# Kernel tuning notes

Measured on AMD Instinct MI355X. Metric: run time of the kernel, lower is better.

Reference implementation:

```python
import jax, jax.numpy as jnp
import numpy as np

N, D_IN, D_OUT = 8192, 1024, 1024

def setup_inputs() -> dict:
    key = jax.random.key(0)
    kx, kq, kk, kv = jax.random.split(key, 4)
    s = 1.0 / np.sqrt(D_IN)
    return {
        "x": jax.random.normal(kx, (N, D_IN), dtype=jnp.float32),
        "W_q": jax.random.normal(kq, (D_OUT, D_IN), dtype=jnp.float32) * s,
        "W_k": jax.random.normal(kk, (D_OUT, D_IN), dtype=jnp.float32) * s,
        "W_v": jax.random.normal(kv, (D_OUT, D_IN), dtype=jnp.float32) * s,
    }

def reference(x, W_q, W_k, W_v):
    # nn.Linear stores weight as [out, in]: y = x @ W.T
    q = x @ W_q.T          # [N, D_OUT]
    k = x @ W_k.T          # [N, D_OUT]
    v = x @ W_v.T          # [N, D_OUT]
    scale = 1.0 / jnp.sqrt(jnp.asarray(k.shape[-1], dtype=x.dtype))
    scores = (q @ k.T) * scale            # [N, N]
    attn = jax.nn.softmax(scores, axis=-1)
    return attn @ v                        # [N, D_OUT]
```

## Files before the change

### kernel.cpp

```cpp
#include <hip/hip_runtime.h>
#include <hip/hip_bf16.h>
#include <cstdint>
#include <cstddef>


typedef __attribute__((ext_vector_type(8))) short short8;
typedef __attribute__((ext_vector_type(8))) unsigned short ushort8;
typedef __attribute__((ext_vector_type(4))) float f32x4;

#define FENCE asm volatile("" ::: "memory")

__device__ __forceinline__ unsigned short f2bf(float f) {
  unsigned u = __float_as_uint(f);
  u += 0x7fffu + ((u >> 16) & 1u);
  return (unsigned short)(u >> 16);
}
__device__ __forceinline__ float bf2f(unsigned short h) {
  return __uint_as_float(((unsigned)h) << 16);
}

__device__ __forceinline__ void glds16(const void* g, void* l) {
  __builtin_amdgcn_global_load_lds((__attribute__((address_space(1))) void*)g,
                                   (__attribute__((address_space(3))) void*)l,
                                   16, 0, 0);
}

__global__ __launch_bounds__(256) void cast_kernel(const float* __restrict__ in,
                                                   unsigned short* __restrict__ out,
                                                   int n8) {
  int i = blockIdx.x * 256 + threadIdx.x;
  if (i >= n8) return;
  const f32x4* in4 = (const f32x4*)in;
  f32x4 a = in4[2 * i];
  f32x4 b = in4[2 * i + 1];
  ushort8 o;
#pragma unroll
  for (int j = 0; j < 4; ++j) o[j] = f2bf(a[j]);
#pragma unroll
  for (int j = 0; j < 4; ++j) o[4 + j] = f2bf(b[j]);
  ((ushort8*)out)[i] = o;
}

#define MFMA_OP(mi, ni, av, bv) \
  acc[mi][ni] = __builtin_amdgcn_mfma_f32_16x16x32_bf16(av, bv, acc[mi][ni], 0, 0, 0)

template <typename OutT>
__device__ __forceinline__ void gemm_core(
    const unsigned short* __restrict__ A, const unsigned short* __restrict__ B,
    OutT* __restrict__ C, int ldc, size_t ldab , int NT,
    int gm0, int gn0, float scale, char* lA, char* lB) {
  const int tid = threadIdx.x;
  const int lane = tid & 63, w = tid >> 6;
  const int wm = w >> 2, wn = w & 3;

  const int rc0 = w * 32 + (lane >> 2);
  const int rc1 = rc0 + 16;
  const int scol = ((lane & 3) << 4) ^ (((lane >> 3) & 3) << 4);
  const char* pA0 = (const char*)A + (size_t)(gm0 + rc0) * ldab + scol;
  const char* pA1 = (const char*)A + (size_t)(gm0 + rc1) * ldab + scol;
  const char* pB0 = (const char*)B + (size_t)(gn0 + rc0) * ldab + scol;
  const char* pB1 = (const char*)B + (size_t)(gn0 + rc1) * ldab + scol;
  char* dA = lA + w * 2048;
  char* dB = lB + w * 2048;

  const int colb = ((lane >> 4) << 4) ^ (((lane >> 1) & 3) << 4);
  const int aoff = (wm * 128 + (lane & 15)) * 64 + colb;
  const int boff = (wn * 64 + (lane & 15)) * 64 + colb;

  f32x4 acc[8][4];
#pragma unroll
  for (int m = 0; m < 8; ++m)
#pragma unroll
    for (int n = 0; n < 4; ++n) acc[m][n] = (f32x4)(0.0f);

  for (int t = 0; t < 2; ++t) {
    glds16(pA0 + (size_t)t * 64, dA + t * 16384);
    glds16(pA1 + (size_t)t * 64, dA + t * 16384 + 1024);
    glds16(pB0 + (size_t)t * 64, dB + t * 16384);
    glds16(pB1 + (size_t)t * 64, dB + t * 16384 + 1024);
  }
  asm volatile("s_waitcnt vmcnt(4)" ::: "memory");
  __builtin_amdgcn_s_barrier();
  FENCE;

  for (int t = 0; t < NT; ++t) {
    const int slot = t & 3;
    const char* As = lA + slot * 16384;
    const char* Bs = lB + slot * 16384;
    const bool stg = (t + 2 < NT);
    const int s2 = (t + 2) & 3;
    const size_t go = (size_t)(t + 2) * 64;
    short8 a0, a1, a2, a3, b0, b1, b2, b3;

    if (stg) glds16(pA0 + go, dA + s2 * 16384);
    a0 = *(const short8*)(As + aoff);
    a1 = *(const short8*)(As + aoff + 1024);
    a2 = *(const short8*)(As + aoff + 2048);
    a3 = *(const short8*)(As + aoff + 3072);
    b0 = *(const short8*)(Bs + boff);
    b1 = *(const short8*)(Bs + boff + 1024);
    __builtin_amdgcn_s_setprio(1);
    MFMA_OP(0, 0, a0, b0); MFMA_OP(0, 1, a0, b1);
    MFMA_OP(1, 0, a1, b0); MFMA_OP(1, 1, a1, b1);
    MFMA_OP(2, 0, a2, b0); MFMA_OP(2, 1, a2, b1);
    MFMA_OP(3, 0, a3, b0); MFMA_OP(3, 1, a3, b1);
    __builtin_amdgcn_s_setprio(0);
    FENCE; __builtin_amdgcn_s_barrier(); FENCE;

    if (stg) glds16(pA1 + go, dA + s2 * 16384 + 1024);
    b2 = *(const short8*)(Bs + boff + 2048);
    b3 = *(const short8*)(Bs + boff + 3072);
    __builtin_amdgcn_s_setprio(1);
    MFMA_OP(0, 2, a0, b2); MFMA_OP(0, 3, a0, b3);
    MFMA_OP(1, 2, a1, b2); MFMA_OP(1, 3, a1, b3);
    MFMA_OP(2, 2, a2, b2); MFMA_OP(2, 3, a2, b3);
    MFMA_OP(3, 2, a3, b2); MFMA_OP(3, 3, a3, b3);
    __builtin_amdgcn_s_setprio(0);
    FENCE; __builtin_amdgcn_s_barrier(); FENCE;

    if (stg) glds16(pB0 + go, dB + s2 * 16384);
    a0 = *(const short8*)(As + aoff + 4096);
    a1 = *(const short8*)(As + aoff + 5120);
    a2 = *(const short8*)(As + aoff + 6144);
    a3 = *(const short8*)(As + aoff + 7168);
    __builtin_amdgcn_s_setprio(1);
    MFMA_OP(4, 0, a0, b0); MFMA_OP(4, 1, a0, b1);
    MFMA_OP(5, 0, a1, b0); MFMA_OP(5, 1, a1, b1);
    MFMA_OP(6, 0, a2, b0); MFMA_OP(6, 1, a2, b1);
    MFMA_OP(7, 0, a3, b0); MFMA_OP(7, 1, a3, b1);
    __builtin_amdgcn_s_setprio(0);
    FENCE; __builtin_amdgcn_s_barrier(); FENCE;

    if (stg) glds16(pB1 + go, dB + s2 * 16384 + 1024);
    __builtin_amdgcn_s_setprio(1);
    MFMA_OP(4, 2, a0, b2); MFMA_OP(4, 3, a0, b3);
    MFMA_OP(5, 2, a1, b2); MFMA_OP(5, 3, a1, b3);
    MFMA_OP(6, 2, a2, b2); MFMA_OP(6, 3, a2, b3);
    MFMA_OP(7, 2, a3, b2); MFMA_OP(7, 3, a3, b3);
    __builtin_amdgcn_s_setprio(0);
    if (stg) asm volatile("s_waitcnt vmcnt(4)" ::: "memory");
    else     asm volatile("s_waitcnt vmcnt(0)" ::: "memory");
    __builtin_amdgcn_s_barrier();
    FENCE;
  }

  const int r0 = gm0 + wm * 128 + ((lane >> 4) << 2);
  const int c0 = gn0 + wn * 64 + (lane & 15);
#pragma unroll
  for (int mi = 0; mi < 8; ++mi) {
#pragma unroll
    for (int ni = 0; ni < 4; ++ni) {
      f32x4 v = acc[mi][ni];
#pragma unroll
      for (int j = 0; j < 4; ++j) {
        float val = v[j] * scale;
        size_t idx = (size_t)(r0 + mi * 16 + j) * ldc + (c0 + ni * 16);
        if (sizeof(OutT) == 2) ((unsigned short*)C)[idx] = f2bf(val);
        else                   ((float*)C)[idx] = val;
      }
    }
  }
}

__device__ __forceinline__ void swz_block(int& bx, int& by, int& bz) {
  const int gx = gridDim.x, gy = gridDim.y;
  const int f = (blockIdx.z * gy + blockIdx.y) * gx + blockIdx.x;
  const int nwg = gx * gy * gridDim.z;
  const int q = nwg >> 3;
  const int l = (f & 7) * q + (f >> 3);
  bx = l % gx;
  const int r = l / gx;
  by = r % gy;
  bz = r / gy;
}

__global__ __launch_bounds__(512, 2) void gemm_s_kernel(
    const unsigned short* __restrict__ Q, const unsigned short* __restrict__ Kh,
    unsigned short* __restrict__ S) {
  __shared__ char lA[4 * 16384];
  __shared__ char lB[4 * 16384];
  int bx, by, bz; swz_block(bx, by, bz);
  gemm_core<unsigned short>(Q, Kh, S, 8192, 2048, 32, by * 256, bx * 256,
                            0.03125f, lA, lB);
}

__global__ __launch_bounds__(512, 2) void gemm_qkv_kernel(
    const unsigned short* __restrict__ X,
    const unsigned short* __restrict__ Wq, const unsigned short* __restrict__ Wk,
    const unsigned short* __restrict__ Wv,
    unsigned short* __restrict__ Qo, unsigned short* __restrict__ Ko,
    unsigned short* __restrict__ Vo) {
  __shared__ char lA[4 * 16384];
  __shared__ char lB[4 * 16384];
  int bx, by, bz; swz_block(bx, by, bz);
  const unsigned short* B = (bz == 0) ? Wq : (bz == 1) ? Wk : Wv;
  unsigned short* C = (bz == 0) ? Qo : (bz == 1) ? Ko : Vo;
  gemm_core<unsigned short>(X, B, C, 1024, 2048, 32, by * 256, bx * 256,
                            1.0f, lA, lB);
}

__global__ __launch_bounds__(512, 2) void gemm_pv_kernel(
    const unsigned short* __restrict__ S, const unsigned short* __restrict__ Vt,
    float* __restrict__ O, float* __restrict__ P1) {
  __shared__ char lA[4 * 16384];
  __shared__ char lB[4 * 16384];
  int bx, by, bz; swz_block(bx, by, bz);
  const unsigned short* A = S + (size_t)bz * 4096;
  const unsigned short* B = Vt + (size_t)bz * 4096;
  float* C = bz ? P1 : O;
  gemm_core<float>(A, B, C, 1024, 16384, 128, by * 256, bx * 256, 1.0f, lA, lB);
}

__global__ __launch_bounds__(256) void add_kernel(float* __restrict__ out,
                                                  const float* __restrict__ p,
                                                  int n4) {
  int i = blockIdx.x * 256 + threadIdx.x;
  if (i < n4) {
    f32x4 a = ((const f32x4*)out)[i];
    f32x4 b = ((const f32x4*)p)[i];
    ((f32x4*)out)[i] = a + b;
  }
}

__global__ __launch_bounds__(256) void softmax_kernel(unsigned short* __restrict__ S,
                                                      int ncol) {
  const int t = threadIdx.x;
  unsigned short* rp = S + (size_t)blockIdx.x * ncol;
  ushort8* rv = (ushort8*)rp;
  float f[32];
#pragma unroll
  for (int c = 0; c < 4; ++c) {
    ushort8 v = rv[c * 256 + t];
#pragma unroll
    for (int j = 0; j < 8; ++j) f[c * 8 + j] = bf2f(v[j]);
  }
  float m = -1e30f;
#pragma unroll
  for (int i = 0; i < 32; ++i) m = fmaxf(m, f[i]);
#pragma unroll
  for (int o = 32; o; o >>= 1) m = fmaxf(m, __shfl_xor(m, o));
  __shared__ float red[8];
  if ((t & 63) == 0) red[t >> 6] = m;
  __syncthreads();
  m = fmaxf(fmaxf(red[0], red[1]), fmaxf(red[2], red[3]));

  float s = 0.0f;
#pragma unroll
  for (int i = 0; i < 32; ++i) {
    f[i] = __expf(f[i] - m);
    s += f[i];
  }
#pragma unroll
  for (int o = 32; o; o >>= 1) s += __shfl_xor(s, o);
  if ((t & 63) == 0) red[4 + (t >> 6)] = s;
  __syncthreads();
  s = red[4] + red[5] + red[6] + red[7];
  float inv = 1.0f / s;
#pragma unroll
  for (int c = 0; c < 4; ++c) {
    ushort8 v;
#pragma unroll
    for (int j = 0; j < 8; ++j) v[j] = f2bf(f[c * 8 + j] * inv);
    rv[c * 256 + t] = v;
  }
}

__global__ __launch_bounds__(256) void transpose_kernel(
    const unsigned short* __restrict__ in, unsigned short* __restrict__ out,
    int R, int Ccols) {
  __shared__ unsigned short tile[64][65];
  const int tx = threadIdx.x & 63, ty = threadIdx.x >> 6;
  const int r0 = blockIdx.y * 64, c0 = blockIdx.x * 64;
#pragma unroll
  for (int i = 0; i < 16; ++i) {
    int r = ty * 16 + i;
    tile[r][tx] = in[(size_t)(r0 + r) * Ccols + c0 + tx];
  }
  __syncthreads();
#pragma unroll
  for (int i = 0; i < 16; ++i) {
    int r = ty * 16 + i;
    out[(size_t)(c0 + r) * R + r0 + tx] = tile[tx][r];
  }
}

extern "C" void kernel_launch(void* const* d_in, const int* in_sizes, int n_in,
                              void* d_out, int out_size, void* d_ws, size_t ws_size,
                              hipStream_t stream) {
  (void)in_sizes; (void)n_in; (void)out_size; (void)ws_size;
  const int N = 8192, D = 1024;
  const float* x  = (const float*)d_in[0];
  const float* Wq = (const float*)d_in[1];
  const float* Wk = (const float*)d_in[2];
  const float* Wv = (const float*)d_in[3];
  float* out = (float*)d_out;

  char* ws = (char*)d_ws;
  size_t off = 0;
  auto alloc = [&](size_t bytes) { char* p = ws + off; off += bytes; return p; };
  unsigned short* xh  = (unsigned short*)alloc((size_t)N * D * 2);
  unsigned short* Wqh = (unsigned short*)alloc((size_t)D * D * 2);
  unsigned short* Wkh = (unsigned short*)alloc((size_t)D * D * 2);
  unsigned short* Wvh = (unsigned short*)alloc((size_t)D * D * 2);
  unsigned short* Qh  = (unsigned short*)alloc((size_t)N * D * 2);
  unsigned short* Kh  = (unsigned short*)alloc((size_t)N * D * 2);
  unsigned short* Vh  = (unsigned short*)alloc((size_t)N * D * 2);
  unsigned short* S   = (unsigned short*)alloc((size_t)N * N * 2);
  unsigned short* Vth = xh;
  float* Pbuf = (float*)Qh;

  cast_kernel<<<(N * D / 8) / 256, 256, 0, stream>>>(x, xh, N * D / 8);
  cast_kernel<<<(D * D / 8) / 256, 256, 0, stream>>>(Wq, Wqh, D * D / 8);
  cast_kernel<<<(D * D / 8) / 256, 256, 0, stream>>>(Wk, Wkh, D * D / 8);
  cast_kernel<<<(D * D / 8) / 256, 256, 0, stream>>>(Wv, Wvh, D * D / 8);

  gemm_qkv_kernel<<<dim3(4, 32, 3), 512, 0, stream>>>(xh, Wqh, Wkh, Wvh,
                                                      Qh, Kh, Vh);

  gemm_s_kernel<<<dim3(32, 32), 512, 0, stream>>>(Qh, Kh, S);

  softmax_kernel<<<N, 256, 0, stream>>>(S, N);

  transpose_kernel<<<dim3(D / 64, N / 64), 256, 0, stream>>>(Vh, Vth, N, D);

  gemm_pv_kernel<<<dim3(4, 32, 2), 512, 0, stream>>>(S, Vth, out, Pbuf);

  add_kernel<<<(N * D / 4) / 256, 256, 0, stream>>>(out, Pbuf, N * D / 4);
}
```

Baseline: 608.9 us.

## Double-buffer 64-wide K tiles with register-prefetched fragments in GEMM core

Reworks the shared GEMM main loop to stage K-tiles of 64 instead of 32, using two LDS buffers of 64 KB each (128 KB total) with a new XOR swizzle. A and B fragments are held in registers in lo/hi halves, and the next A fragment is prefetched before the final MFMA quad. This halves the number of outer iterations and the barrier overhead per K element. The S-GEMM output is also written with nontemporal stores so the large score matrix bypasses cache. In exchange the kernel uses much more LDS, which may rule out two blocks per CU despite launch_bounds(512,2), and adds register pressure and extra barriers.

```diff
diff --git a/kernel.cpp b/kernel.cpp
--- a/kernel.cpp
+++ b/kernel.cpp
@@ -9,6 +9,9 @@
 typedef __attribute__((ext_vector_type(4))) float f32x4;
 
 #define FENCE asm volatile("" ::: "memory")
+__device__ __forceinline__ void wgbar() {
+  FENCE; __builtin_amdgcn_s_barrier(); FENCE;
+}
 
 __device__ __forceinline__ unsigned short f2bf(float f) {
   unsigned u = __float_as_uint(f);
@@ -41,31 +44,40 @@
   ((ushort8*)out)[i] = o;
 }
 
-#define MFMA_OP(mi, ni, av, bv) \
-  acc[mi][ni] = __builtin_amdgcn_mfma_f32_16x16x32_bf16(av, bv, acc[mi][ni], 0, 0, 0)
-
-template <typename OutT>
+#define QUAD(mbase, nbase, aArr, bArr)                                        \
+  do {                                                                        \
+    _Pragma("unroll") for (int m_ = 0; m_ < 4; ++m_)                          \
+    _Pragma("unroll") for (int n_ = 0; n_ < 2; ++n_)                          \
+    _Pragma("unroll") for (int k_ = 0; k_ < 2; ++k_)                          \
+      acc[(mbase) + m_][(nbase) + n_] =                                       \
+        __builtin_amdgcn_mfma_f32_16x16x32_bf16(aArr[m_][k_], bArr[n_][k_],   \
+          acc[(mbase) + m_][(nbase) + n_], 0, 0, 0);                          \
+  } while (0)
+
+template <typename OutT, bool NTS>
 __device__ __forceinline__ void gemm_core(
     const unsigned short* __restrict__ A, const unsigned short* __restrict__ B,
-    OutT* __restrict__ C, int ldc, size_t ldab , int NT,
-    int gm0, int gn0, float scale, char* lA, char* lB) {
+    OutT* __restrict__ C, int ldc, size_t ldab , int NT2,
+    int gm0, int gn0, float scale, char* lds) {
   const int tid = threadIdx.x;
   const int lane = tid & 63, w = tid >> 6;
   const int wm = w >> 2, wn = w & 3;
 
-  const int rc0 = w * 32 + (lane >> 2);
-  const int rc1 = rc0 + 16;
-  const int scol = ((lane & 3) << 4) ^ (((lane >> 3) & 3) << 4);
-  const char* pA0 = (const char*)A + (size_t)(gm0 + rc0) * ldab + scol;
-  const char* pA1 = (const char*)A + (size_t)(gm0 + rc1) * ldab + scol;
-  const char* pB0 = (const char*)B + (size_t)(gn0 + rc0) * ldab + scol;
-  const char* pB1 = (const char*)B + (size_t)(gn0 + rc1) * ldab + scol;
-  char* dA = lA + w * 2048;
-  char* dB = lB + w * 2048;
-
-  const int colb = ((lane >> 4) << 4) ^ (((lane >> 1) & 3) << 4);
-  const int aoff = (wm * 128 + (lane & 15)) * 64 + colb;
-  const int boff = (wn * 64 + (lane & 15)) * 64 + colb;
+  char* const A0b = lds;
+  char* const B0b = lds + 32768;
+  char* const A1b = lds + 65536;
+  char* const B1b = lds + 65536 + 32768;
+
+  const size_t off64 = (size_t)64 * ldab;
+  const int scol = (((tid & 7) ^ ((tid >> 3) & 7)) << 4);
+  const char* pAs = (const char*)A + (size_t)(gm0 + (tid >> 3)) * ldab + scol;
+  const char* pBs = (const char*)B + (size_t)(gn0 + (tid >> 3)) * ldab + scol;
+  const int dstw = w * 1024;
+
+  const int aRd = wm * 16384 + (lane & 15) * 128;
+  const int bRd = wn * 8192 + (lane & 15) * 128;
+  const int kc0 = (((lane >> 4) << 4) ^ ((lane & 7) << 4));
+  const int kc1 = kc0 ^ 64;
 
   f32x4 acc[8][4];
 #pragma unroll
@@ -73,75 +85,97 @@
 #pragma unroll
     for (int n = 0; n < 4; ++n) acc[m][n] = (f32x4)(0.0f);
 
-  for (int t = 0; t < 2; ++t) {
-    glds16(pA0 + (size_t)t * 64, dA + t * 16384);
-    glds16(pA1 + (size_t)t * 64, dA + t * 16384 + 1024);
-    glds16(pB0 + (size_t)t * 64, dB + t * 16384);
-    glds16(pB1 + (size_t)t * 64, dB + t * 16384 + 1024);
-  }
+  short8 aLo[4][2], aHi[4][2], bLo[2][2], bHi[2][2];
+
+#pragma unroll
+  for (int c = 0; c < 4; ++c) glds16(pAs + c * off64, A0b + c * 8192 + dstw);
+#pragma unroll
+  for (int c = 0; c < 4; ++c) glds16(pBs + c * off64, B0b + c * 8192 + dstw);
   asm volatile("s_waitcnt vmcnt(4)" ::: "memory");
-  __builtin_amdgcn_s_barrier();
-  FENCE;
-
-  for (int t = 0; t < NT; ++t) {
-    const int slot = t & 3;
-    const char* As = lA + slot * 16384;
-    const char* Bs = lB + slot * 16384;
-    const bool stg = (t + 2 < NT);
-    const int s2 = (t + 2) & 3;
-    const size_t go = (size_t)(t + 2) * 64;
-    short8 a0, a1, a2, a3, b0, b1, b2, b3;
-
-    if (stg) glds16(pA0 + go, dA + s2 * 16384);
-    a0 = *(const short8*)(As + aoff);
-    a1 = *(const short8*)(As + aoff + 1024);
-    a2 = *(const short8*)(As + aoff + 2048);
-    a3 = *(const short8*)(As + aoff + 3072);
-    b0 = *(const short8*)(Bs + boff);
-    b1 = *(const short8*)(Bs + boff + 1024);
+  wgbar();
+#pragma unroll
+  for (int m = 0; m < 4; ++m) {
+    aLo[m][0] = *(const short8*)(A0b + aRd + m * 2048 + kc0);
+    aLo[m][1] = *(const short8*)(A0b + aRd + m * 2048 + kc1);
+  }
+
+  const char* sA = pAs + 128;
+  const char* sB = pBs + 128;
+
+  for (int j = 0; j < NT2; ++j) {
+    const int par = j & 1;
+    const char* Ab = par ? A1b : A0b;
+    const char* Bb = par ? B1b : B0b;
+    char* An = par ? A0b : A1b;
+    char* Bn = par ? B0b : B1b;
+    const bool stg = (j + 1 < NT2);
+
+    if (stg) {
+      glds16(sA, An + dstw);
+      glds16(sA + off64, An + 8192 + dstw);
+    }
+    if (stg) asm volatile("s_waitcnt vmcnt(2)" ::: "memory");
+    else     asm volatile("s_waitcnt vmcnt(0)" ::: "memory");
+    wgbar();
+#pragma unroll
+    for (int n = 0; n < 2; ++n) {
+      bLo[n][0] = *(const short8*)(Bb + bRd + n * 2048 + kc0);
+      bLo[n][1] = *(const short8*)(Bb + bRd + n * 2048 + kc1);
+    }
     __builtin_amdgcn_s_setprio(1);
-    MFMA_OP(0, 0, a0, b0); MFMA_OP(0, 1, a0, b1);
-    MFMA_OP(1, 0, a1, b0); MFMA_OP(1, 1, a1, b1);
-    MFMA_OP(2, 0, a2, b0); MFMA_OP(2, 1, a2, b1);
-    MFMA_OP(3, 0, a3, b0); MFMA_OP(3, 1, a3, b1);
+    QUAD(0, 0, aLo, bLo);
     __builtin_amdgcn_s_setprio(0);
-    FENCE; __builtin_amdgcn_s_barrier(); FENCE;
-
-    if (stg) glds16(pA1 + go, dA + s2 * 16384 + 1024);
-    b2 = *(const short8*)(Bs + boff + 2048);
-    b3 = *(const short8*)(Bs + boff + 3072);
+    wgbar();
+
+    if (stg) {
+      glds16(sA + 2 * off64, An + 16384 + dstw);
+      glds16(sA + 3 * off64, An + 24576 + dstw);
+    }
+#pragma unroll
+    for (int n = 0; n < 2; ++n) {
+      bHi[n][0] = *(const short8*)(Bb + bRd + (2 + n) * 2048 + kc0);
+      bHi[n][1] = *(const short8*)(Bb + bRd + (2 + n) * 2048 + kc1);
+    }
+    wgbar();
     __builtin_amdgcn_s_setprio(1);
-    MFMA_OP(0, 2, a0, b2); MFMA_OP(0, 3, a0, b3);
-    MFMA_OP(1, 2, a1, b2); MFMA_OP(1, 3, a1, b3);
-    MFMA_OP(2, 2, a2, b2); MFMA_OP(2, 3, a2, b3);
-    MFMA_OP(3, 2, a3, b2); MFMA_OP(3, 3, a3, b3);
+    QUAD(0, 2, aLo, bHi);
     __builtin_amdgcn_s_setprio(0);
-    FENCE; __builtin_amdgcn_s_barrier(); FENCE;
-
-    if (stg) glds16(pB0 + go, dB + s2 * 16384);
-    a0 = *(const short8*)(As + aoff + 4096);
-    a1 = *(const short8*)(As + aoff + 5120);
-    a2 = *(const short8*)(As + aoff + 6144);
-    a3 = *(const short8*)(As + aoff + 7168);
+    wgbar();
+
+    if (stg) {
+      glds16(sB, Bn + dstw);
+      glds16(sB + off64, Bn + 8192 + dstw);
+    }
+#pragma unroll
+    for (int m = 0; m < 4; ++m) {
+      aHi[m][0] = *(const short8*)(Ab + aRd + (4 + m) * 2048 + kc0);
+      aHi[m][1] = *(const short8*)(Ab + aRd + (4 + m) * 2048 + kc1);
+    }
+    wgbar();
     __builtin_amdgcn_s_setprio(1);
-    MFMA_OP(4, 0, a0, b0); MFMA_OP(4, 1, a0, b1);
-    MFMA_OP(5, 0, a1, b0); MFMA_OP(5, 1, a1, b1);
-    MFMA_OP(6, 0, a2, b0); MFMA_OP(6, 1, a2, b1);
-    MFMA_OP(7, 0, a3, b0); MFMA_OP(7, 1, a3, b1);
+    QUAD(4, 2, aHi, bHi);
     __builtin_amdgcn_s_setprio(0);
-    FENCE; __builtin_amdgcn_s_barrier(); FENCE;
-
-    if (stg) glds16(pB1 + go, dB + s2 * 16384 + 1024);
+    wgbar();
+
+    if (stg) {
+      glds16(sB + 2 * off64, Bn + 16384 + dstw);
+      glds16(sB + 3 * off64, Bn + 24576 + dstw);
+      asm volatile("s_waitcnt vmcnt(4)" ::: "memory");
+    }
+    wgbar();
+    if (stg) {
+#pragma unroll
+      for (int m = 0; m < 4; ++m) {
+        aLo[m][0] = *(const short8*)(An + aRd + m * 2048 + kc0);
+        aLo[m][1] = *(const short8*)(An + aRd + m * 2048 + kc1);
+      }
+    }
     __builtin_amdgcn_s_setprio(1);
-    MFMA_OP(4, 2, a0, b2); MFMA_OP(4, 3, a0, b3);
-    MFMA_OP(5, 2, a1, b2); MFMA_OP(5, 3, a1, b3);
-    MFMA_OP(6, 2, a2, b2); MFMA_OP(6, 3, a2, b3);
-    MFMA_OP(7, 2, a3, b2); MFMA_OP(7, 3, a3, b3);
+    QUAD(4, 0, aHi, bLo);
     __builtin_amdgcn_s_setprio(0);
-    if (stg) asm volatile("s_waitcnt vmcnt(4)" ::: "memory");
-    else     asm volatile("s_waitcnt vmcnt(0)" ::: "memory");
-    __builtin_amdgcn_s_barrier();
-    FENCE;
+    wgbar();
+
+    sA += 128; sB += 128;
   }
 
   const int r0 = gm0 + wm * 128 + ((lane >> 4) << 2);
@@ -152,11 +186,16 @@
     for (int ni = 0; ni < 4; ++ni) {
       f32x4 v = acc[mi][ni];
 #pragma unroll
-      for (int j = 0; j < 4; ++j) {
-        float val = v[j] * scale;
-        size_t idx = (size_t)(r0 + mi * 16 + j) * ldc + (c0 + ni * 16);
-        if (sizeof(OutT) == 2) ((unsigned short*)C)[idx] = f2bf(val);
-        else                   ((float*)C)[idx] = val;
+      for (int jj = 0; jj < 4; ++jj) {
+        float val = v[jj] * scale;
+        size_t idx = (size_t)(r0 + mi * 16 + jj) * ldc + (c0 + ni * 16);
+        if (sizeof(OutT) == 2) {
+          unsigned short hv = f2bf(val);
+          if (NTS) __builtin_nontemporal_store(hv, (unsigned short*)C + idx);
+          else     ((unsigned short*)C)[idx] = hv;
+        } else {
+          ((float*)C)[idx] = val;
+        }
       }
     }
   }
@@ -177,11 +216,10 @@
 __global__ __launch_bounds__(512, 2) void gemm_s_kernel(
     const unsigned short* __restrict__ Q, const unsigned short* __restrict__ Kh,
     unsigned short* __restrict__ S) {
-  __shared__ char lA[4 * 16384];
-  __shared__ char lB[4 * 16384];
+  __shared__ char lds[131072];
   int bx, by, bz; swz_block(bx, by, bz);
-  gemm_core<unsigned short>(Q, Kh, S, 8192, 2048, 32, by * 256, bx * 256,
-                            0.03125f, lA, lB);
+  gemm_core<unsigned short, true>(Q, Kh, S, 8192, 2048, 16, by * 256, bx * 256,
+                                  0.03125f, lds);
 }
 
 __global__ __launch_bounds__(512, 2) void gemm_qkv_kernel(
@@ -190,25 +228,24 @@
     const unsigned short* __restrict__ Wv,
     unsigned short* __restrict__ Qo, unsigned short* __restrict__ Ko,
     unsigned short* __restrict__ Vo) {
-  __shared__ char lA[4 * 16384];
-  __shared__ char lB[4 * 16384];
+  __shared__ char lds[131072];
   int bx, by, bz; swz_block(bx, by, bz);
   const unsigned short* B = (bz == 0) ? Wq : (bz == 1) ? Wk : Wv;
   unsigned short* C = (bz == 0) ? Qo : (bz == 1) ? Ko : Vo;
-  gemm_core<unsigned short>(X, B, C, 1024, 2048, 32, by * 256, bx * 256,
-                            1.0f, lA, lB);
+  gemm_core<unsigned short, false>(X, B, C, 1024, 2048, 16, by * 256, bx * 256,
+                                   1.0f, lds);
 }
 
 __global__ __launch_bounds__(512, 2) void gemm_pv_kernel(
     const unsigned short* __restrict__ S, const unsigned short* __restrict__ Vt,
     float* __restrict__ O, float* __restrict__ P1) {
-  __shared__ char lA[4 * 16384];
-  __shared__ char lB[4 * 16384];
+  __shared__ char lds[131072];
   int bx, by, bz; swz_block(bx, by, bz);
   const unsigned short* A = S + (size_t)bz * 4096;
   const unsigned short* B = Vt + (size_t)bz * 4096;
   float* C = bz ? P1 : O;
-  gemm_core<float>(A, B, C, 1024, 16384, 128, by * 256, bx * 256, 1.0f, lA, lB);
+  gemm_core<float, false>(A, B, C, 1024, 16384, 64, by * 256, bx * 256,
+                          1.0f, lds);
 }
 
 __global__ __launch_bounds__(256) void add_kernel(float* __restrict__ out,
```

New measurement: 510.6 us. 1.19x faster.
